# Kernel tuning notes

Hardware: AMD Instinct MI355X
Metric: run time of the kernel (lower is better)

Reference implementation:

```python
import jax, jax.numpy as jnp
import numpy as np

N = 50000       # nodes
E = 800000      # edges
D = 64          # node_feats
H = 4           # heads
NEG_SLOPE = 0.2
LN_EPS = 1e-5


def setup_inputs() -> dict:
    key = jax.random.key(0)
    ks = jax.random.split(key, 8)
    h = jax.random.normal(ks[0], (N, D), dtype=jnp.float32)
    src = jax.random.randint(ks[1], (E,), 0, N, dtype=jnp.int32)
    dst = jax.random.randint(ks[2], (E,), 0, N, dtype=jnp.int32)
    # parameters (kaiming-uniform-ish scaling)
    W_node = jax.random.normal(ks[3], (D, H * D), dtype=jnp.float32) * (1.0 / np.sqrt(D))
    b_node = jnp.zeros((H * D,), dtype=jnp.float32)
    att = jax.random.normal(ks[4], (H, 2 * D), dtype=jnp.float32) * (1.0 / np.sqrt(2 * D))
    W_scale = jax.random.normal(ks[5], (H * D, D), dtype=jnp.float32) * (1.0 / np.sqrt(H * D))
    bias = jnp.zeros((D,), dtype=jnp.float32)
    ln_gamma = jnp.ones((D,), dtype=jnp.float32)
    ln_beta = jnp.zeros((D,), dtype=jnp.float32)
    return {"h": h, "src": src, "dst": dst, "W_node": W_node, "b_node": b_node,
            "att": att, "W_scale": W_scale, "bias": bias,
            "ln_gamma": ln_gamma, "ln_beta": ln_beta}


def reference(h, src, dst, W_node, b_node, att, W_scale, bias, ln_gamma, ln_beta):
    n, d = h.shape
    heads = att.shape[0]
    # node linear projection -> [N, H, D]
    wv = (h @ W_node + b_node).reshape(n, heads, d)
    u = wv[src]            # [E, H, D] source features (messages)
    v = wv[dst]            # [E, H, D] destination features
    a_u, a_v = att[:, :d], att[:, d:]
    # attention logit per edge/head: sum(cat(u,v) * a)
    logit = jnp.einsum('ehd,hd->eh', u, a_u) + jnp.einsum('ehd,hd->eh', v, a_v)
    logit = jax.nn.leaky_relu(logit, NEG_SLOPE)
    # segment softmax over incoming edges of each dst node
    smax = jax.ops.segment_max(logit, dst, num_segments=n)        # [N, H]
    smax = jnp.where(jnp.isfinite(smax), smax, 0.0)               # nodes w/o in-edges
    ex = jnp.exp(logit - smax[dst])                               # [E, H]
    denom = jax.ops.segment_sum(ex, dst, num_segments=n)          # [N, H]
    agg = jax.ops.segment_sum(ex[:, :, None] * u, dst, num_segments=n)  # [N, H, D]
    agg = agg / jnp.maximum(denom, 1e-16)[:, :, None]
    # scale back to node_feats, residual, layernorm, relu (dropout = eval identity)
    h_new = agg.reshape(n, heads * d) @ W_scale + bias
    x = h_new + h
    mu = jnp.mean(x, axis=-1, keepdims=True)
    var = jnp.var(x, axis=-1, keepdims=True)
    xn = (x - mu) * jax.lax.rsqrt(var + LN_EPS)
    return jax.nn.relu(xn * ln_gamma + ln_beta)
```

## Files before the change

### kernel.cpp

```cpp
#include <hip/hip_runtime.h>
#include <hip/hip_fp16.h>

#define N_NODES 50000
#define N_EDGES 800000
#define NEG_SLOPE 0.2f
#define LN_EPS 1e-5f
#define ALPHA_BLOCKS 1024
#define H1_BLOCKS 3125
#define NB1 391
#define NB1P 392

typedef _Float16 f16;
typedef f16 f16x4 __attribute__((ext_vector_type(4)));
typedef f16 f16x8 __attribute__((ext_vector_type(8)));
typedef float f32x4 __attribute__((ext_vector_type(4)));

__global__ __launch_bounds__(256) void k_pre(
    const float* __restrict__ Wn, const float* __restrict__ bn,
    const float* __restrict__ att, const float* __restrict__ Ws,
    const float* __restrict__ bias,
    float* __restrict__ qu, float* __restrict__ qv, float* __restrict__ cuv,
    f16* __restrict__ Mt16, float* __restrict__ cvec)
{
    const int b = blockIdx.x, t = threadIdx.x;
    if (b < 64) {
        int e = b * 256 + t;
        int hd = e >> 12, k = (e >> 6) & 63, c = e & 63;
        float s = 0.f;
        for (int j = 0; j < 64; ++j)
            s = fmaf(Wn[k * 256 + hd * 64 + j], Ws[(hd * 64 + j) * 64 + c], s);
        Mt16[c * 256 + hd * 64 + k] = (f16)s;
    } else if (b == 64) {
        int hd = t >> 6, k = t & 63;
        float su = 0.f, sv = 0.f;
        for (int j = 0; j < 64; ++j) {
            float w = Wn[k * 256 + hd * 64 + j];
            su = fmaf(w, att[hd * 128 + j], su);
            sv = fmaf(w, att[hd * 128 + 64 + j], sv);
        }
        qu[hd * 64 + k] = su;
        qv[hd * 64 + k] = sv;
        if (t < 8) {
            int hh = t & 3;
            const float* a = att + hh * 128 + (t >> 2) * 64;
            float s = 0.f;
            for (int j = 0; j < 64; ++j) s = fmaf(bn[hh * 64 + j], a[j], s);
            cuv[t] = s;
        }
    } else {
        if (t < 64) {
            float s = bias[t];
            for (int kk = 0; kk < 256; ++kk) s = fmaf(bn[kk], Ws[kk * 64 + t], s);
            cvec[t] = s;
        }
    }
}

__global__ __launch_bounds__(256) void k_front3(
    const float* __restrict__ h, const int* __restrict__ dst,
    const float* __restrict__ qu, const float* __restrict__ qv, const float* __restrict__ cuv,
    __half* __restrict__ h16, float* __restrict__ alpha_u, float* __restrict__ alpha_v,
    int* __restrict__ g)
{
    __shared__ int hist[NB1P];
    const int t = threadIdx.x;
    if (blockIdx.x >= ALPHA_BLOCKS) {
        const int blk = blockIdx.x - ALPHA_BLOCKS;
        for (int i = t; i < NB1P; i += 256) hist[i] = 0;
        __syncthreads();
        const int e = blk * 256 + t;
        atomicAdd(&hist[dst[e] >> 7], 1);
        __syncthreads();
        for (int i = t; i < NB1P; i += 256) g[blk * NB1P + i] = hist[i];
        return;
    }
    const int lane = t & 63;
    const int wid = blockIdx.x * 4 + (t >> 6);
    const float qur0 = qu[lane], qur1 = qu[64 + lane], qur2 = qu[128 + lane], qur3 = qu[192 + lane];
    const float qvr0 = qv[lane], qvr1 = qv[64 + lane], qvr2 = qv[128 + lane], qvr3 = qv[192 + lane];
    const float4 cu = *(const float4*)cuv;
    const float4 cv = *(const float4*)(cuv + 4);
    for (int n = wid; n < N_NODES; n += ALPHA_BLOCKS * 4) {
        float hv = h[(size_t)n * 64 + lane];
        h16[(size_t)n * 64 + lane] = __float2half(hv);
        float pu0 = hv * qur0, pu1 = hv * qur1, pu2 = hv * qur2, pu3 = hv * qur3;
        float pv0 = hv * qvr0, pv1 = hv * qvr1, pv2 = hv * qvr2, pv3 = hv * qvr3;
#pragma unroll
        for (int off = 32; off; off >>= 1) {
            pu0 += __shfl_xor(pu0, off);
            pu1 += __shfl_xor(pu1, off);
            pu2 += __shfl_xor(pu2, off);
            pu3 += __shfl_xor(pu3, off);
            pv0 += __shfl_xor(pv0, off);
            pv1 += __shfl_xor(pv1, off);
            pv2 += __shfl_xor(pv2, off);
            pv3 += __shfl_xor(pv3, off);
        }
        if (lane == 0) {
            *(float4*)(alpha_u + n * 4) = make_float4(pu0 + cu.x, pu1 + cu.y, pu2 + cu.z, pu3 + cu.w);
            *(float4*)(alpha_v + n * 4) = make_float4(pv0 + cv.x, pv1 + cv.y, pv2 + cv.z, pv3 + cv.w);
        }
    }
}

__device__ __forceinline__ int wave_incl_scan(int x, int lane) {
#pragma unroll
    for (int off = 1; off < 64; off <<= 1) {
        int y = __shfl_up(x, off);
        if (lane >= off) x += y;
    }
    return x;
}

__global__ __launch_bounds__(64) void k_s1(const int* __restrict__ g,
                                           int* __restrict__ off1, int* __restrict__ tot) {
    const int b = blockIdx.x;
    const int lane = threadIdx.x;
    int running = 0;
    for (int c = 0; c < H1_BLOCKS; c += 64) {
        const int blk = c + lane;
        int v = (blk < H1_BLOCKS) ? g[blk * NB1P + b] : 0;
        int incl = wave_incl_scan(v, lane);
        if (blk < H1_BLOCKS) off1[blk * NB1P + b] = running + incl - v;
        running += __shfl(incl, 63);
    }
    if (lane == 0) tot[b] = running;
}

__global__ __launch_bounds__(64) void k_base(const int* __restrict__ tot, int* __restrict__ base) {
    const int lane = threadIdx.x;
    int running = 0;
    for (int c = 0; c < NB1P; c += 64) {
        const int i = c + lane;
        int v = (i < NB1) ? tot[i] : 0;
        int incl = wave_incl_scan(v, lane);
        if (i < NB1P) base[i] = running + incl - v;
        running += __shfl(incl, 63);
    }
}

__global__ __launch_bounds__(256) void k_h1scat(
    const int* __restrict__ src, const int* __restrict__ dst,
    const int* __restrict__ base, const int* __restrict__ off1,
    int* __restrict__ ebuf)
{
    __shared__ int cur[NB1P];
    const int t = threadIdx.x;
    const int blk = blockIdx.x;
    for (int i = t; i < NB1P; i += 256)
        cur[i] = (i < NB1) ? base[i] + off1[blk * NB1P + i] : 0;
    __syncthreads();
    const int e = blk * 256 + t;
    const int s = src[e], d = dst[e];
    const int pos = atomicAdd(&cur[d >> 7], 1);
    ebuf[pos] = (s << 7) | (d & 127);
}

__global__ __launch_bounds__(256) void k_h2(
    const int* __restrict__ ebuf, const int* __restrict__ base,
    const float* __restrict__ alpha_u, const float* __restrict__ alpha_v,
    int* __restrict__ rowptr, int* __restrict__ csr_src, float* __restrict__ csr_w)
{
    __shared__ int hist[128], lscan[128], cur[128];
    const int t = threadIdx.x;
    const int b = blockIdx.x;
    const int r0 = base[b], r1 = base[b + 1];
    if (t < 128) hist[t] = 0;
    __syncthreads();
    for (int j = r0 + t; j < r1; j += 256) atomicAdd(&hist[ebuf[j] & 127], 1);
    __syncthreads();
    if (t < 64) {
        int running = 0;
        for (int c = 0; c < 128; c += 64) {
            int v = hist[c + t];
            int incl = wave_incl_scan(v, t);
            lscan[c + t] = running + incl - v;
            running += __shfl(incl, 63);
        }
    }
    __syncthreads();
    if (t < 128) {
        const int n = b * 128 + t;
        if (n <= N_NODES) rowptr[n] = r0 + lscan[t];
        cur[t] = lscan[t];
    }
    __syncthreads();
    for (int j = r0 + t; j < r1; j += 256) {
        const int p = ebuf[j];
        const int dl = p & 127, s = p >> 7;
        const int pos = r0 + atomicAdd(&cur[dl], 1);
        const int d = b * 128 + dl;
        const float4 au = *(const float4*)(alpha_u + (size_t)s * 4);
        const float4 av = *(const float4*)(alpha_v + (size_t)d * 4);
        float l0 = au.x + av.x; l0 = l0 > 0.f ? l0 : NEG_SLOPE * l0;
        float l1 = au.y + av.y; l1 = l1 > 0.f ? l1 : NEG_SLOPE * l1;
        float l2 = au.z + av.z; l2 = l2 > 0.f ? l2 : NEG_SLOPE * l2;
        float l3 = au.w + av.w; l3 = l3 > 0.f ? l3 : NEG_SLOPE * l3;
        csr_src[pos] = s;
        *(float4*)(csr_w + (size_t)pos * 4) =
            make_float4(__expf(l0), __expf(l1), __expf(l2), __expf(l3));
    }
}

__global__ __launch_bounds__(256) void k_agg3(
    const int* __restrict__ rowptr, const int* __restrict__ csr_src,
    const float* __restrict__ csr_w, const __half* __restrict__ h16,
    f16* __restrict__ aggh16, int n0, int n1)
{
    const int lane = threadIdx.x & 63;
    const int wid = (blockIdx.x * 256 + threadIdx.x) >> 6;
    const int nwaves = (gridDim.x * 256) >> 6;
    for (int n = n0 + wid; n < n1; n += nwaves) {
        const int r0 = rowptr[n], r1 = rowptr[n + 1];
        float d0 = 0.f, d1 = 0.f, d2 = 0.f, d3 = 0.f;
        float a0 = 0.f, a1 = 0.f, a2 = 0.f, a3 = 0.f;
        const int rlast = r1 - 1;
        for (int j = r0; j < r1; j += 8) {
            int jdx[8], s[8];
#pragma unroll
            for (int i = 0; i < 8; ++i) {
                int jj = j + i;
                jdx[i] = jj < rlast ? jj : rlast;
                s[i] = __builtin_amdgcn_readfirstlane(csr_src[jdx[i]]);
            }
            float hv[8];
#pragma unroll
            for (int i = 0; i < 8; ++i)
                hv[i] = __half2float(h16[(size_t)s[i] * 64 + lane]);
            float4 w[8];
#pragma unroll
            for (int i = 0; i < 8; ++i)
                w[i] = *(const float4*)(csr_w + (size_t)jdx[i] * 4);
#pragma unroll
            for (int i = 0; i < 8; ++i) {
                const bool valid = (j + i < r1);
                float e0 = valid ? w[i].x : 0.f;
                float e1 = valid ? w[i].y : 0.f;
                float e2 = valid ? w[i].z : 0.f;
                float e3 = valid ? w[i].w : 0.f;
                d0 += e0; a0 = fmaf(e0, hv[i], a0);
                d1 += e1; a1 = fmaf(e1, hv[i], a1);
                d2 += e2; a2 = fmaf(e2, hv[i], a2);
                d3 += e3; a3 = fmaf(e3, hv[i], a3);
            }
        }
        const float i0 = 1.0f / fmaxf(d0, 1e-16f);
        const float i1 = 1.0f / fmaxf(d1, 1e-16f);
        const float i2 = 1.0f / fmaxf(d2, 1e-16f);
        const float i3 = 1.0f / fmaxf(d3, 1e-16f);
        f16* __restrict__ arow = aggh16 + (size_t)n * 256;
        arow[lane]       = (f16)(a0 * i0);
        arow[64 + lane]  = (f16)(a1 * i1);
        arow[128 + lane] = (f16)(a2 * i2);
        arow[192 + lane] = (f16)(a3 * i3);
    }
}

__global__ __launch_bounds__(256) void k_post_mfma(
    const f16* __restrict__ aggh16, const f16* __restrict__ Mt16,
    const float* __restrict__ cvec, const float* __restrict__ h,
    const float* __restrict__ gamma_, const float* __restrict__ beta_,
    float* __restrict__ out)
{
    __shared__ f16 Mlds[64 * 256];
    const int t = threadIdx.x;
    {
        const uint4* g = (const uint4*)Mt16;
        uint4* l = (uint4*)Mlds;
#pragma unroll
        for (int i = 0; i < 8; ++i) {
            int ch = i * 256 + t;
            l[ch ^ ((ch >> 5) & 7)] = g[ch];
        }
    }
    __syncthreads();
    const int lane = t & 63;
    const int l15 = lane & 15, lg = lane >> 4;
    float cv_r[4], ga_r[4], be_r[4];
#pragma unroll
    for (int ct = 0; ct < 4; ++ct) {
        int c = ct * 16 + l15;
        cv_r[ct] = cvec[c]; ga_r[ct] = gamma_[c]; be_r[ct] = beta_[c];
    }
    const int wid0 = (blockIdx.x * 256 + t) >> 6;
    const int nw = (gridDim.x * 256) >> 6;
    for (int blk = wid0; blk < N_NODES / 16; blk += nw) {
        f32x4 acc[4] = {{0.f,0.f,0.f,0.f},{0.f,0.f,0.f,0.f},{0.f,0.f,0.f,0.f},{0.f,0.f,0.f,0.f}};
        const f16* arow = aggh16 + (size_t)(blk * 16 + l15) * 256 + 4 * lg;
#pragma unroll
        for (int ks = 0; ks < 8; ++ks) {
            f16x4 alo = *(const f16x4*)(arow + ks * 32);
            f16x4 ahi = *(const f16x4*)(arow + ks * 32 + 16);
            f16x8 a;
            a[0]=alo[0]; a[1]=alo[1]; a[2]=alo[2]; a[3]=alo[3];
            a[4]=ahi[0]; a[5]=ahi[1]; a[6]=ahi[2]; a[7]=ahi[3];
#pragma unroll
            for (int ct = 0; ct < 4; ++ct) {
                const int c = ct * 16 + l15;
                const int sw = (c & 7) << 3;
                const int u0 = (c * 256 + ks * 32 + 4 * lg);
                f16x4 blo = *(const f16x4*)(Mlds + (u0 ^ sw));
                f16x4 bhi = *(const f16x4*)(Mlds + ((u0 + 16) ^ sw));
                f16x8 b;
                b[0]=blo[0]; b[1]=blo[1]; b[2]=blo[2]; b[3]=blo[3];
                b[4]=bhi[0]; b[5]=bhi[1]; b[6]=bhi[2]; b[7]=bhi[3];
                acc[ct] = __builtin_amdgcn_mfma_f32_16x16x32_f16(a, b, acc[ct], 0, 0, 0);
            }
        }
#pragma unroll
        for (int e = 0; e < 4; ++e) {
            const int gr = blk * 16 + 4 * lg + e;
            float x[4];
            float s = 0.f;
#pragma unroll
            for (int ct = 0; ct < 4; ++ct) {
                x[ct] = acc[ct][e] + cv_r[ct] + h[(size_t)gr * 64 + ct * 16 + l15];
                s += x[ct];
            }
            s += __shfl_xor(s, 1); s += __shfl_xor(s, 2);
            s += __shfl_xor(s, 4); s += __shfl_xor(s, 8);
            const float mu = s * (1.0f / 64.0f);
            float v = 0.f;
#pragma unroll
            for (int ct = 0; ct < 4; ++ct) { float d = x[ct] - mu; v = fmaf(d, d, v); }
            v += __shfl_xor(v, 1); v += __shfl_xor(v, 2);
            v += __shfl_xor(v, 4); v += __shfl_xor(v, 8);
            const float rinv = rsqrtf(v * (1.0f / 64.0f) + LN_EPS);
#pragma unroll
            for (int ct = 0; ct < 4; ++ct) {
                float xn = (x[ct] - mu) * rinv;
                out[(size_t)gr * 64 + ct * 16 + l15] = fmaxf(xn * ga_r[ct] + be_r[ct], 0.0f);
            }
        }
    }
}

extern "C" void kernel_launch(void* const* d_in, const int* in_sizes, int n_in,
                              void* d_out, int out_size, void* d_ws, size_t ws_size,
                              hipStream_t stream) {
    const float* h      = (const float*)d_in[0];
    const int*   src    = (const int*)d_in[1];
    const int*   dst    = (const int*)d_in[2];
    const float* Wn     = (const float*)d_in[3];
    const float* bn     = (const float*)d_in[4];
    const float* att    = (const float*)d_in[5];
    const float* Ws     = (const float*)d_in[6];
    const float* bias   = (const float*)d_in[7];
    const float* gamma_ = (const float*)d_in[8];
    const float* beta_  = (const float*)d_in[9];
    float* out = (float*)d_out;

    char* ws = (char*)d_ws;
    size_t off = 0;
    auto alloc = [&](size_t bytes) { void* p = ws + off; off = (off + bytes + 255) & ~(size_t)255; return p; };
    __half* h16    = (__half*)alloc((size_t)N_NODES * 64 * 2);
    f16*   aggh16  = (f16*)alloc((size_t)N_NODES * 256 * 2);
    float* alpha_u = (float*)alloc((size_t)N_NODES * 4 * 4);
    float* alpha_v = (float*)alloc((size_t)N_NODES * 4 * 4);
    int*   rowptr  = (int*)alloc((size_t)(N_NODES + 1) * 4);
    int*   csr_src = (int*)alloc((size_t)N_EDGES * 4);
    float* csr_w   = (float*)alloc((size_t)N_EDGES * 4 * 4);
    int*   g       = (int*)alloc((size_t)H1_BLOCKS * NB1P * 4);
    int*   off1    = (int*)alloc((size_t)H1_BLOCKS * NB1P * 4);
    int*   tot     = (int*)alloc((size_t)NB1P * 4);
    int*   base    = (int*)alloc((size_t)(NB1P + 1) * 4);
    int*   ebuf    = (int*)alloc((size_t)N_EDGES * 4);
    float* qu      = (float*)alloc(256 * 4);
    float* qv      = (float*)alloc(256 * 4);
    float* cuv     = (float*)alloc(8 * 4);
    f16*   Mt16    = (f16*)alloc(16384 * 2);
    float* cvec    = (float*)alloc(64 * 4);

    k_pre<<<66, 256, 0, stream>>>(Wn, bn, att, Ws, bias, qu, qv, cuv, Mt16, cvec);
    k_front3<<<ALPHA_BLOCKS + H1_BLOCKS, 256, 0, stream>>>(h, dst, qu, qv, cuv,
                                                           h16, alpha_u, alpha_v, g);
    k_s1<<<NB1, 64, 0, stream>>>(g, off1, tot);
    k_base<<<1, 64, 0, stream>>>(tot, base);
    k_h1scat<<<H1_BLOCKS, 256, 0, stream>>>(src, dst, base, off1, ebuf);
    k_h2<<<NB1, 256, 0, stream>>>(ebuf, base, alpha_u, alpha_v, rowptr, csr_src, csr_w);
    k_agg3<<<2048, 256, 0, stream>>>(rowptr, csr_src, csr_w, h16, aggh16, 0, 12500);
    k_agg3<<<2048, 256, 0, stream>>>(rowptr, csr_src, csr_w, h16, aggh16, 12500, 25000);
    k_agg3<<<2048, 256, 0, stream>>>(rowptr, csr_src, csr_w, h16, aggh16, 25000, 37500);
    k_agg3<<<2048, 256, 0, stream>>>(rowptr, csr_src, csr_w, h16, aggh16, 37500, N_NODES);
    k_post_mfma<<<782, 256, 0, stream>>>(aggh16, Mt16, cvec, h, gamma_, beta_, out);
}
```

Before: 263.1 us.

## Merge preprocessing kernels, fold base scan into consumers, coarsen histogram blocks

Merges k_pre and k_front3 into one kernel. Each alpha block now recomputes the qu/qv/cuv projections into shared memory instead of reading them from a separate launch. The k_base launch is removed and every k_h1scat and k_h2 block recomputes the small prefix scan of bucket totals. Histogram/scatter blocks now handle 512 edges each, halving the g/off1 arrays and the k_s1 scan length, k_s1 packs 4 waves per block, and the four k_agg3 launches become one. The aim is to cut kernel launches and intermediate traffic, at the cost of redundant per-block recomputation.

```diff
diff --git a/kernel.cpp b/kernel.cpp
--- a/kernel.cpp
+++ b/kernel.cpp
@@ -6,7 +6,9 @@
 #define NEG_SLOPE 0.2f
 #define LN_EPS 1e-5f
 #define ALPHA_BLOCKS 1024
-#define H1_BLOCKS 3125
+#define PRE_BLOCKS 65
+#define EPB 512
+#define HB 1563
 #define NB1 391
 #define NB1P 392
 
@@ -15,14 +17,27 @@
 typedef f16 f16x8 __attribute__((ext_vector_type(8)));
 typedef float f32x4 __attribute__((ext_vector_type(4)));
 
-__global__ __launch_bounds__(256) void k_pre(
-    const float* __restrict__ Wn, const float* __restrict__ bn,
-    const float* __restrict__ att, const float* __restrict__ Ws,
-    const float* __restrict__ bias,
-    float* __restrict__ qu, float* __restrict__ qv, float* __restrict__ cuv,
-    f16* __restrict__ Mt16, float* __restrict__ cvec)
-{
+__device__ __forceinline__ int wave_incl_scan(int x, int lane) {
+#pragma unroll
+    for (int off = 1; off < 64; off <<= 1) {
+        int y = __shfl_up(x, off);
+        if (lane >= off) x += y;
+    }
+    return x;
+}
+
+__global__ __launch_bounds__(256) void k_mega1(
+    const float* __restrict__ h, const float* __restrict__ Wn,
+    const float* __restrict__ bn, const float* __restrict__ att,
+    const float* __restrict__ Ws, const float* __restrict__ bias,
+    const int* __restrict__ dst,
+    __half* __restrict__ h16, float* __restrict__ alpha_u, float* __restrict__ alpha_v,
+    f16* __restrict__ Mt16, float* __restrict__ cvec, int* __restrict__ g)
+{
+    __shared__ float squ[256], sqv[256], scuv[8];
+    __shared__ int shist[NB1P];
     const int b = blockIdx.x, t = threadIdx.x;
+
     if (b < 64) {
         int e = b * 256 + t;
         int hd = e >> 12, k = (e >> 6) & 63, c = e & 63;
@@ -30,56 +45,53 @@
         for (int j = 0; j < 64; ++j)
             s = fmaf(Wn[k * 256 + hd * 64 + j], Ws[(hd * 64 + j) * 64 + c], s);
         Mt16[c * 256 + hd * 64 + k] = (f16)s;
-    } else if (b == 64) {
-        int hd = t >> 6, k = t & 63;
-        float su = 0.f, sv = 0.f;
-        for (int j = 0; j < 64; ++j) {
-            float w = Wn[k * 256 + hd * 64 + j];
-            su = fmaf(w, att[hd * 128 + j], su);
-            sv = fmaf(w, att[hd * 128 + 64 + j], sv);
-        }
-        qu[hd * 64 + k] = su;
-        qv[hd * 64 + k] = sv;
-        if (t < 8) {
-            int hh = t & 3;
-            const float* a = att + hh * 128 + (t >> 2) * 64;
-            float s = 0.f;
-            for (int j = 0; j < 64; ++j) s = fmaf(bn[hh * 64 + j], a[j], s);
-            cuv[t] = s;
-        }
-    } else {
+        return;
+    }
+    if (b == 64) {
         if (t < 64) {
             float s = bias[t];
             for (int kk = 0; kk < 256; ++kk) s = fmaf(bn[kk], Ws[kk * 64 + t], s);
             cvec[t] = s;
         }
-    }
-}
-
-__global__ __launch_bounds__(256) void k_front3(
-    const float* __restrict__ h, const int* __restrict__ dst,
-    const float* __restrict__ qu, const float* __restrict__ qv, const float* __restrict__ cuv,
-    __half* __restrict__ h16, float* __restrict__ alpha_u, float* __restrict__ alpha_v,
-    int* __restrict__ g)
-{
-    __shared__ int hist[NB1P];
-    const int t = threadIdx.x;
-    if (blockIdx.x >= ALPHA_BLOCKS) {
-        const int blk = blockIdx.x - ALPHA_BLOCKS;
-        for (int i = t; i < NB1P; i += 256) hist[i] = 0;
+        return;
+    }
+    if (b >= PRE_BLOCKS + ALPHA_BLOCKS) {
+        const int blk = b - (PRE_BLOCKS + ALPHA_BLOCKS);
+        for (int i = t; i < NB1P; i += 256) shist[i] = 0;
         __syncthreads();
-        const int e = blk * 256 + t;
-        atomicAdd(&hist[dst[e] >> 7], 1);
+        const int e0 = blk * EPB;
+        const int e1 = (e0 + EPB < N_EDGES) ? e0 + EPB : N_EDGES;
+        for (int e = e0 + t; e < e1; e += 256) atomicAdd(&shist[dst[e] >> 7], 1);
         __syncthreads();
-        for (int i = t; i < NB1P; i += 256) g[blk * NB1P + i] = hist[i];
+        for (int i = t; i < NB1P; i += 256) g[blk * NB1P + i] = shist[i];
         return;
     }
+    {
+        const int hd = t >> 6, k = t & 63;
+        const float* wrow = Wn + k * 256 + hd * 64;
+        const float* arow = att + hd * 128;
+        float su = 0.f, sv = 0.f;
+        for (int j = 0; j < 64; ++j) {
+            float w = wrow[j];
+            su = fmaf(w, arow[j], su);
+            sv = fmaf(w, arow[64 + j], sv);
+        }
+        squ[t] = su; sqv[t] = sv;
+        if (t < 8) {
+            int hh = t & 3;
+            const float* a2 = att + hh * 128 + (t >> 2) * 64;
+            float s = 0.f;
+            for (int j = 0; j < 64; ++j) s = fmaf(bn[hh * 64 + j], a2[j], s);
+            scuv[t] = s;
+        }
+    }
+    __syncthreads();
     const int lane = t & 63;
-    const int wid = blockIdx.x * 4 + (t >> 6);
-    const float qur0 = qu[lane], qur1 = qu[64 + lane], qur2 = qu[128 + lane], qur3 = qu[192 + lane];
-    const float qvr0 = qv[lane], qvr1 = qv[64 + lane], qvr2 = qv[128 + lane], qvr3 = qv[192 + lane];
-    const float4 cu = *(const float4*)cuv;
-    const float4 cv = *(const float4*)(cuv + 4);
+    const int wid = (b - PRE_BLOCKS) * 4 + (t >> 6);
+    const float qur0 = squ[lane], qur1 = squ[64 + lane], qur2 = squ[128 + lane], qur3 = squ[192 + lane];
+    const float qvr0 = sqv[lane], qvr1 = sqv[64 + lane], qvr2 = sqv[128 + lane], qvr3 = sqv[192 + lane];
+    const float4 cu = make_float4(scuv[0], scuv[1], scuv[2], scuv[3]);
+    const float4 cv = make_float4(scuv[4], scuv[5], scuv[6], scuv[7]);
     for (int n = wid; n < N_NODES; n += ALPHA_BLOCKS * 4) {
         float hv = h[(size_t)n * 64 + lane];
         h16[(size_t)n * 64 + lane] = __float2half(hv);
@@ -103,68 +115,75 @@
     }
 }
 
-__device__ __forceinline__ int wave_incl_scan(int x, int lane) {
-#pragma unroll
-    for (int off = 1; off < 64; off <<= 1) {
-        int y = __shfl_up(x, off);
-        if (lane >= off) x += y;
-    }
-    return x;
-}
-
-__global__ __launch_bounds__(64) void k_s1(const int* __restrict__ g,
-                                           int* __restrict__ off1, int* __restrict__ tot) {
-    const int b = blockIdx.x;
-    const int lane = threadIdx.x;
+__global__ __launch_bounds__(256) void k_s1(const int* __restrict__ g,
+                                            int* __restrict__ off1, int* __restrict__ tot) {
+    const int b = blockIdx.x * 4 + (threadIdx.x >> 6);
+    const int lane = threadIdx.x & 63;
+    if (b >= NB1) return;
     int running = 0;
-    for (int c = 0; c < H1_BLOCKS; c += 64) {
+    for (int c = 0; c < HB; c += 64) {
         const int blk = c + lane;
-        int v = (blk < H1_BLOCKS) ? g[blk * NB1P + b] : 0;
+        int v = (blk < HB) ? g[blk * NB1P + b] : 0;
         int incl = wave_incl_scan(v, lane);
-        if (blk < H1_BLOCKS) off1[blk * NB1P + b] = running + incl - v;
+        if (blk < HB) off1[blk * NB1P + b] = running + incl - v;
         running += __shfl(incl, 63);
     }
     if (lane == 0) tot[b] = running;
-}
-
-__global__ __launch_bounds__(64) void k_base(const int* __restrict__ tot, int* __restrict__ base) {
-    const int lane = threadIdx.x;
-    int running = 0;
-    for (int c = 0; c < NB1P; c += 64) {
-        const int i = c + lane;
-        int v = (i < NB1) ? tot[i] : 0;
-        int incl = wave_incl_scan(v, lane);
-        if (i < NB1P) base[i] = running + incl - v;
-        running += __shfl(incl, 63);
-    }
 }
 
 __global__ __launch_bounds__(256) void k_h1scat(
     const int* __restrict__ src, const int* __restrict__ dst,
-    const int* __restrict__ base, const int* __restrict__ off1,
+    const int* __restrict__ tot, const int* __restrict__ off1,
     int* __restrict__ ebuf)
 {
-    __shared__ int cur[NB1P];
+    __shared__ int sbase[NB1P], cur[NB1P];
     const int t = threadIdx.x;
     const int blk = blockIdx.x;
+    if (t < 64) {
+        int running = 0;
+        for (int c = 0; c < NB1P; c += 64) {
+            int i = c + t;
+            int v = (i < NB1) ? tot[i] : 0;
+            int incl = wave_incl_scan(v, t);
+            sbase[i] = running + incl - v;
+            running += __shfl(incl, 63);
+        }
+    }
+    __syncthreads();
     for (int i = t; i < NB1P; i += 256)
-        cur[i] = (i < NB1) ? base[i] + off1[blk * NB1P + i] : 0;
-    __syncthreads();
-    const int e = blk * 256 + t;
-    const int s = src[e], d = dst[e];
-    const int pos = atomicAdd(&cur[d >> 7], 1);
-    ebuf[pos] = (s << 7) | (d & 127);
+        cur[i] = (i < NB1) ? sbase[i] + off1[blk * NB1P + i] : 0;
+    __syncthreads();
+    const int e0 = blk * EPB;
+    const int e1 = (e0 + EPB < N_EDGES) ? e0 + EPB : N_EDGES;
+    for (int e = e0 + t; e < e1; e += 256) {
+        const int s = src[e], d = dst[e];
+        const int pos = atomicAdd(&cur[d >> 7], 1);
+        ebuf[pos] = (s << 7) | (d & 127);
+    }
 }
 
 __global__ __launch_bounds__(256) void k_h2(
-    const int* __restrict__ ebuf, const int* __restrict__ base,
+    const int* __restrict__ ebuf, const int* __restrict__ tot,
     const float* __restrict__ alpha_u, const float* __restrict__ alpha_v,
     int* __restrict__ rowptr, int* __restrict__ csr_src, float* __restrict__ csr_w)
 {
+    __shared__ int sbase[NB1P + 1];
     __shared__ int hist[128], lscan[128], cur[128];
     const int t = threadIdx.x;
     const int b = blockIdx.x;
-    const int r0 = base[b], r1 = base[b + 1];
+    if (t < 64) {
+        int running = 0;
+        for (int c = 0; c < NB1P; c += 64) {
+            int i = c + t;
+            int v = (i < NB1) ? tot[i] : 0;
+            int incl = wave_incl_scan(v, t);
+            sbase[i] = running + incl - v;
+            running += __shfl(incl, 63);
+        }
+        if (t == 0) sbase[NB1P] = N_EDGES;
+    }
+    __syncthreads();
+    const int r0 = sbase[b], r1 = sbase[b + 1];
     if (t < 128) hist[t] = 0;
     __syncthreads();
     for (int j = r0 + t; j < r1; j += 256) atomicAdd(&hist[ebuf[j] & 127], 1);
@@ -202,15 +221,15 @@
     }
 }
 
-__global__ __launch_bounds__(256) void k_agg3(
+__global__ __launch_bounds__(256) void k_agg(
     const int* __restrict__ rowptr, const int* __restrict__ csr_src,
     const float* __restrict__ csr_w, const __half* __restrict__ h16,
-    f16* __restrict__ aggh16, int n0, int n1)
+    f16* __restrict__ aggh16)
 {
     const int lane = threadIdx.x & 63;
     const int wid = (blockIdx.x * 256 + threadIdx.x) >> 6;
     const int nwaves = (gridDim.x * 256) >> 6;
-    for (int n = n0 + wid; n < n1; n += nwaves) {
+    for (int n = wid; n < N_NODES; n += nwaves) {
         const int r0 = rowptr[n], r1 = rowptr[n + 1];
         float d0 = 0.f, d1 = 0.f, d2 = 0.f, d3 = 0.f;
         float a0 = 0.f, a1 = 0.f, a2 = 0.f, a3 = 0.f;
@@ -360,27 +379,18 @@
     int*   rowptr  = (int*)alloc((size_t)(N_NODES + 1) * 4);
     int*   csr_src = (int*)alloc((size_t)N_EDGES * 4);
     float* csr_w   = (float*)alloc((size_t)N_EDGES * 4 * 4);
-    int*   g       = (int*)alloc((size_t)H1_BLOCKS * NB1P * 4);
-    int*   off1    = (int*)alloc((size_t)H1_BLOCKS * NB1P * 4);
+    int*   g       = (int*)alloc((size_t)HB * NB1P * 4);
+    int*   off1    = (int*)alloc((size_t)HB * NB1P * 4);
     int*   tot     = (int*)alloc((size_t)NB1P * 4);
-    int*   base    = (int*)alloc((size_t)(NB1P + 1) * 4);
     int*   ebuf    = (int*)alloc((size_t)N_EDGES * 4);
-    float* qu      = (float*)alloc(256 * 4);
-    float* qv      = (float*)alloc(256 * 4);
-    float* cuv     = (float*)alloc(8 * 4);
     f16*   Mt16    = (f16*)alloc(16384 * 2);
     float* cvec    = (float*)alloc(64 * 4);
 
-    k_pre<<<66, 256, 0, stream>>>(Wn, bn, att, Ws, bias, qu, qv, cuv, Mt16, cvec);
-    k_front3<<<ALPHA_BLOCKS + H1_BLOCKS, 256, 0, stream>>>(h, dst, qu, qv, cuv,
-                                                           h16, alpha_u, alpha_v, g);
-    k_s1<<<NB1, 64, 0, stream>>>(g, off1, tot);
-    k_base<<<1, 64, 0, stream>>>(tot, base);
-    k_h1scat<<<H1_BLOCKS, 256, 0, stream>>>(src, dst, base, off1, ebuf);
-    k_h2<<<NB1, 256, 0, stream>>>(ebuf, base, alpha_u, alpha_v, rowptr, csr_src, csr_w);
-    k_agg3<<<2048, 256, 0, stream>>>(rowptr, csr_src, csr_w, h16, aggh16, 0, 12500);
-    k_agg3<<<2048, 256, 0, stream>>>(rowptr, csr_src, csr_w, h16, aggh16, 12500, 25000);
-    k_agg3<<<2048, 256, 0, stream>>>(rowptr, csr_src, csr_w, h16, aggh16, 25000, 37500);
-    k_agg3<<<2048, 256, 0, stream>>>(rowptr, csr_src, csr_w, h16, aggh16, 37500, N_NODES);
+    k_mega1<<<PRE_BLOCKS + ALPHA_BLOCKS + HB, 256, 0, stream>>>(
+        h, Wn, bn, att, Ws, bias, dst, h16, alpha_u, alpha_v, Mt16, cvec, g);
+    k_s1<<<98, 256, 0, stream>>>(g, off1, tot);
+    k_h1scat<<<HB, 256, 0, stream>>>(src, dst, tot, off1, ebuf);
+    k_h2<<<NB1, 256, 0, stream>>>(ebuf, tot, alpha_u, alpha_v, rowptr, csr_src, csr_w);
+    k_agg<<<2048, 256, 0, stream>>>(rowptr, csr_src, csr_w, h16, aggh16);
     k_post_mfma<<<782, 256, 0, stream>>>(aggh16, Mt16, cvec, h, gamma_, beta_, out);
 }
```

New measurement: 236.9 us. 1.11x faster.
